# Performance work log

Measured on AMD Instinct MI355X. Metric: run time of the kernel, lower is better.

Reference implementation:

```python
import jax, jax.numpy as jnp
import numpy as np

BIG = 1.0e6  # cost for empty groups
EPS = 1e-6

COST_ACTIVITY = 1.0
COST_GROUP = 1.0
COST_SIZE = 1.0


def setup_inputs() -> dict:
    key = jax.random.key(0)
    k1, k2, k3, k4 = jax.random.split(key, 4)
    bs, Q, C = 256, 512, 128   # batch, num_queries, num_activity_classes
    P, G = 256, 128            # num_persons, num_target_groups
    return {
        "pred_activity_logits": jax.random.normal(k1, (bs, Q, C), dtype=jnp.float32),
        "attention_logits": jax.random.normal(k2, (bs, P, Q), dtype=jnp.float32),
        "tgt_activity_ids": jax.random.randint(k3, (bs, G), 0, C),
        "tgt_group_ids": jax.random.randint(k4, (bs, P), 0, G),
    }


def reference(pred_activity_logits, attention_logits, tgt_activity_ids, tgt_group_ids):
    bs, Q, C = pred_activity_logits.shape
    P = attention_logits.shape[1]
    G = tgt_activity_ids.shape[1]

    # out_attw_b.T -> [Q, P]; log_softmax over dim 0 (queries)
    attw = jnp.transpose(attention_logits, (0, 2, 1))          # [bs, Q, P]
    logP = jax.nn.log_softmax(attw, axis=1)                    # softmax over queries
    P_qn = jnp.exp(logP)
    P_clamped = jnp.clip(P_qn, EPS, 1.0 - EPS)
    lognegP = jnp.log1p(-P_clamped)                            # [bs, Q, P]

    # one-hot grouping target: M[b, p, g] = 1 iff person p in group g
    M = jax.nn.one_hot(tgt_group_ids, G, dtype=logP.dtype)     # [bs, P, G]
    m = M.sum(axis=1)                                          # [bs, G] members per group
    nm = P - m                                                 # nonmembers per group

    # grouping cost: -mean member logP - mean nonmember log(1-P)
    mem_sum = jnp.einsum('bqp,bpg->bqg', logP, M)
    non_sum = jnp.einsum('bqp,bpg->bqg', lognegP, 1.0 - M)
    safe_m = jnp.maximum(m, 1.0)[:, None, :]
    safe_nm = jnp.maximum(nm, 1.0)[:, None, :]
    grouping_cost = -mem_sum / safe_m - non_sum / safe_nm      # [bs, Q, G]

    # size cost: |sum_p P_qn - m| / n_person
    pred_size = P_qn.sum(axis=2)                               # [bs, Q]
    size_cost = jnp.abs(pred_size[:, :, None] - m[:, None, :]) / max(float(P), 1.0)

    empty = (m == 0)[:, None, :]                               # [bs, 1, G]
    grouping_cost = jnp.where(empty, BIG, grouping_cost)
    size_cost = jnp.where(empty, BIG, size_cost)

    # activity cost: cross-entropy of query logits vs each group's activity class
    logq = jax.nn.log_softmax(pred_activity_logits, axis=-1)   # [bs, Q, C]
    idx = jnp.broadcast_to(tgt_activity_ids[:, None, :], (bs, Q, G))
    activity_cost = -jnp.take_along_axis(logq, idx, axis=2)    # [bs, Q, G]

    cost = (COST_GROUP * grouping_cost
            + COST_ACTIVITY * activity_cost
            + COST_SIZE * size_cost)
    return cost
```

## Files before the change

kernel.cpp:

```cpp
#include <hip/hip_runtime.h>

#define BS 256
#define NQ 512
#define NC 128
#define NP 256
#define NG 128
#define TQ 32
#define PTS (NC + 1)
#define BIGC 1.0e6f
#define EPSC 1e-6f


__global__ __launch_bounds__(512) void pre_kernel(const float* __restrict__ att,
                                                  float* __restrict__ lse,
                                                  float* __restrict__ part) {
    __shared__ float attS[32 * NQ];
    __shared__ float invS[32];
    const int t   = threadIdx.x;
    const int blk = blockIdx.x;
    const int b   = blk >> 3;
    const int r   = t >> 4;
    const int p   = (blk & 7) * 32 + r;
    const int sub = t & 15;

    const float4* a4 = (const float4*)(att + ((size_t)(b * NP + p)) * NQ);
    float4 v[8];
#pragma unroll
    for (int i = 0; i < 8; ++i) v[i] = a4[sub + 16 * i];

    float mx = -1e30f;
#pragma unroll
    for (int i = 0; i < 8; ++i)
        mx = fmaxf(mx, fmaxf(fmaxf(v[i].x, v[i].y), fmaxf(v[i].z, v[i].w)));
#pragma unroll
    for (int off = 1; off < 16; off <<= 1) mx = fmaxf(mx, __shfl_xor(mx, off, 64));

    float s = 0.f;
#pragma unroll
    for (int i = 0; i < 8; ++i) {
        v[i].x = __expf(v[i].x - mx); v[i].y = __expf(v[i].y - mx);
        v[i].z = __expf(v[i].z - mx); v[i].w = __expf(v[i].w - mx);
        s += v[i].x + v[i].y + v[i].z + v[i].w;
        *(float4*)(attS + r * NQ + 4 * sub + 64 * i) = v[i];
    }
#pragma unroll
    for (int off = 1; off < 16; off <<= 1) s += __shfl_xor(s, off, 64);
    if (sub == 0) {
        invS[r] = 1.f / s;
        lse[b * NP + p] = mx + __logf(s);
    }
    __syncthreads();

    float sz = 0.f, sl = 0.f;
#pragma unroll 8
    for (int pp = 0; pp < 32; ++pp) {
        const float P = attS[pp * NQ + t] * invS[pp];
        sz += P;
        const float c = fminf(fmaxf(P, EPSC), 1.f - EPSC);
        sl += __logf(1.f - c);
    }
    float* basep = part + (size_t)blk * 2 * NQ;
    basep[t]      = sz;
    basep[NQ + t] = sl;
}

__global__ __launch_bounds__(512, 6) void cost_kernel(
    const float* __restrict__ predAct,
    const float* __restrict__ att,
    const int*   __restrict__ actIds,
    const int*   __restrict__ grpIds,
    const float* __restrict__ lseAtt,
    const float* __restrict__ part,
    float*       __restrict__ out)
{
    __shared__ float wS[NP * TQ];
    __shared__ float pTile[TQ * PTS];
    __shared__ float lseS[NP];
    __shared__ float lseAct[TQ];
    __shared__ float szG[TQ], slG[TQ];
    __shared__ int   gidS[NP];
    __shared__ int   rankS[NP];
    __shared__ int   aidS[NG];
    __shared__ int   cntS[NG];
    __shared__ int   startS[NG];

    const int b  = blockIdx.x >> 4;
    const int q0 = (blockIdx.x & 15) * TQ;
    const int t  = threadIdx.x;

    const int pr  = t >> 3;
    const int qo4 = (t & 7) * 4;
    float4 v[4];
#pragma unroll
    for (int it = 0; it < 4; ++it)
        v[it] = *(const float4*)(att + ((size_t)(b * NP + it * 64 + pr)) * NQ + q0 + qo4);

    const int wv = t >> 6, ln = t & 63;
    float pa0[4], pa1[4];
#pragma unroll
    for (int k = 0; k < 4; ++k) {
        const float* rowp = predAct + ((size_t)(b * NQ + q0 + wv + 8 * k)) * NC;
        pa0[k] = rowp[ln]; pa1[k] = rowp[ln + 64];
    }

    if (t < NP) { lseS[t] = lseAtt[b * NP + t]; gidS[t] = grpIds[b * NP + t]; }
    if (t < NG) { aidS[t] = actIds[b * NG + t]; cntS[t] = 0; }
    if (t < 2 * TQ) {
        const int qo = t & 31, which = t >> 5;
        const float* pb = part + ((size_t)(b * 8)) * 2 * NQ + (size_t)which * NQ + q0 + qo;
        float s = 0.f;
#pragma unroll
        for (int k = 0; k < 8; ++k) s += pb[(size_t)k * 2 * NQ];
        if (which == 0) szG[qo] = s; else slG[qo] = s;
    }
    __syncthreads();

    int myPos = 0;
    if (t < NP) myPos = atomicAdd(&cntS[gidS[t]], 1);
    __syncthreads();

    if (t < 64) {
        const int c0 = cntS[2 * t], c1 = cntS[2 * t + 1];
        const int ps = c0 + c1;
        int s = ps;
#pragma unroll
        for (int off = 1; off < 64; off <<= 1) {
            const int w = __shfl_up(s, off, 64);
            if (t >= off) s += w;
        }
        startS[2 * t]     = s - ps;
        startS[2 * t + 1] = s - ps + c0;
    }
    __syncthreads();
    if (t < NP) rankS[t] = startS[gidS[t]] + myPos;
    __syncthreads();

    #pragma unroll
    for (int it = 0; it < 4; ++it) {
        const int p  = it * 64 + pr;
        const float l = lseS[p];
        const int rr = rankS[p];
        const int m  = cntS[gidS[p]];
        const float im  = 1.f / (float)m;
        const float inm = 1.f / fmaxf((float)(NP - m), 1.f);
        float w[4];
        const float vv[4] = {v[it].x, v[it].y, v[it].z, v[it].w};
#pragma unroll
        for (int j = 0; j < 4; ++j) {
            const float x = vv[j] - l;
            const float e = __expf(x);
            const float c = fminf(fmaxf(e, EPSC), 1.f - EPSC);
            const float ll = __logf(1.f - c);
            w[j] = ll * inm - x * im;
        }
        *(float4*)(wS + rr * TQ + qo4) = *(float4*)w;
    }

#pragma unroll
    for (int k = 0; k < 4; ++k) {
        const int r = wv + 8 * k;
        float mx = fmaxf(pa0[k], pa1[k]);
#pragma unroll
        for (int off = 1; off < 64; off <<= 1) mx = fmaxf(mx, __shfl_xor(mx, off, 64));
        float s = __expf(pa0[k] - mx) + __expf(pa1[k] - mx);
#pragma unroll
        for (int off = 1; off < 64; off <<= 1) s += __shfl_xor(s, off, 64);
        if (ln == 0) lseAct[r] = mx + __logf(s);
        pTile[r * PTS + ln]      = pa0[k];
        pTile[r * PTS + 64 + ln] = pa1[k];
    }
    __syncthreads();

#pragma unroll
    for (int rep = 0; rep < 2; ++rep) {
        const int idx = rep * 512 + t;
        const int qo  = idx & 31;
        const int g4  = (idx >> 5) * 4;
        const float sl = slG[qo], pz = szG[qo], la = lseAct[qo];
        float res[4];
#pragma unroll
        for (int j = 0; j < 4; ++j) {
            const int g  = g4 + j;
            const int m  = cntS[g];
            const int st = startS[g];
            float s = 0.f;
            for (int i = 0; i < m; ++i) s += wS[(st + i) * TQ + qo];
            const float mf  = (float)m;
            const float nmf = fmaxf((float)(NP - m), 1.f);
            float grp = s - sl / nmf;
            float szc = fabsf(pz - mf) * (1.f / (float)NP);
            if (m == 0) { grp = BIGC; szc = BIGC; }
            const float av = pTile[qo * PTS + aidS[g]];
            res[j] = grp + (la - av) + szc;
        }
        *(float4*)(out + ((size_t)(b * NQ + q0 + qo)) * NG + g4) = *(float4*)res;
    }
}

extern "C" void kernel_launch(void* const* d_in, const int* in_sizes, int n_in,
                              void* d_out, int out_size, void* d_ws, size_t ws_size,
                              hipStream_t stream) {
    const float* predAct = (const float*)d_in[0];
    const float* att     = (const float*)d_in[1];
    const int*   actIds  = (const int*)d_in[2];
    const int*   grpIds  = (const int*)d_in[3];
    float*       out     = (float*)d_out;
    float*       lse     = (float*)d_ws;
    float*       part    = lse + (size_t)BS * NP;

    pre_kernel<<<BS * 8, 512, 0, stream>>>(att, lse, part);
    cost_kernel<<<BS * (NQ / TQ), 512, 0, stream>>>(predAct, att, actIds, grpIds, lse, part, out);
}
```

Baseline: 313.7 us.

## Replace per-group member loops with prefix-sum differences and halve pre_kernel LDS

The cost kernel now computes an exclusive prefix sum over the group-sorted weight rows in shared memory, so each group's member sum is a difference of two entries rather than a variable-length loop. Group start and count are packed into one int, and several shared arrays are merged into a scratch buffer to cut LDS use. The pre kernel stages probabilities in two halves through a 16-row buffer, normalising in registers, which halves its LDS and allows more resident blocks. Prefix-sum differences can add float cancellation error, and the pre kernel gains extra barriers.

```diff
diff --git a/kernel.cpp b/kernel.cpp
--- a/kernel.cpp
+++ b/kernel.cpp
@@ -11,11 +11,10 @@
 #define EPSC 1e-6f
 
 
-__global__ __launch_bounds__(512) void pre_kernel(const float* __restrict__ att,
-                                                  float* __restrict__ lse,
-                                                  float* __restrict__ part) {
-    __shared__ float attS[32 * NQ];
-    __shared__ float invS[32];
+__global__ __launch_bounds__(512, 8) void pre_kernel(const float* __restrict__ att,
+                                                     float* __restrict__ lse,
+                                                     float* __restrict__ part) {
+    __shared__ float attS[16 * NQ];
     const int t   = threadIdx.x;
     const int blk = blockIdx.x;
     const int b   = blk >> 3;
@@ -41,24 +40,45 @@
         v[i].x = __expf(v[i].x - mx); v[i].y = __expf(v[i].y - mx);
         v[i].z = __expf(v[i].z - mx); v[i].w = __expf(v[i].w - mx);
         s += v[i].x + v[i].y + v[i].z + v[i].w;
-        *(float4*)(attS + r * NQ + 4 * sub + 64 * i) = v[i];
     }
 #pragma unroll
     for (int off = 1; off < 16; off <<= 1) s += __shfl_xor(s, off, 64);
-    if (sub == 0) {
-        invS[r] = 1.f / s;
-        lse[b * NP + p] = mx + __logf(s);
-    }
-    __syncthreads();
+    const float inv = 1.f / s;
+    if (sub == 0) lse[b * NP + p] = mx + __logf(s);
+#pragma unroll
+    for (int i = 0; i < 8; ++i) {
+        v[i].x *= inv; v[i].y *= inv; v[i].z *= inv; v[i].w *= inv;
+    }
 
     float sz = 0.f, sl = 0.f;
-#pragma unroll 8
-    for (int pp = 0; pp < 32; ++pp) {
-        const float P = attS[pp * NQ + t] * invS[pp];
+    if (r < 16) {
+#pragma unroll
+        for (int i = 0; i < 8; ++i)
+            *(float4*)(attS + r * NQ + 4 * sub + 64 * i) = v[i];
+    }
+    __syncthreads();
+#pragma unroll
+    for (int pp = 0; pp < 16; ++pp) {
+        const float P = attS[pp * NQ + t];
         sz += P;
         const float c = fminf(fmaxf(P, EPSC), 1.f - EPSC);
         sl += __logf(1.f - c);
     }
+    __syncthreads();
+    if (r >= 16) {
+#pragma unroll
+        for (int i = 0; i < 8; ++i)
+            *(float4*)(attS + (r - 16) * NQ + 4 * sub + 64 * i) = v[i];
+    }
+    __syncthreads();
+#pragma unroll
+    for (int pp = 0; pp < 16; ++pp) {
+        const float P = attS[pp * NQ + t];
+        sz += P;
+        const float c = fminf(fmaxf(P, EPSC), 1.f - EPSC);
+        sl += __logf(1.f - c);
+    }
+
     float* basep = part + (size_t)blk * 2 * NQ;
     basep[t]      = sz;
     basep[NQ + t] = sl;
@@ -73,16 +93,17 @@
     const float* __restrict__ part,
     float*       __restrict__ out)
 {
-    __shared__ float wS[NP * TQ];
+    __shared__ float wS[(NP + 1) * TQ];
     __shared__ float pTile[TQ * PTS];
-    __shared__ float lseS[NP];
+    __shared__ float scratch[512];
     __shared__ float lseAct[TQ];
     __shared__ float szG[TQ], slG[TQ];
-    __shared__ int   gidS[NP];
-    __shared__ int   rankS[NP];
     __shared__ int   aidS[NG];
     __shared__ int   cntS[NG];
-    __shared__ int   startS[NG];
+
+    float* lseS  = scratch;
+    int*   prS   = (int*)(scratch + 256);
+    float* scanP = scratch;
 
     const int b  = blockIdx.x >> 4;
     const int q0 = (blockIdx.x & 15) * TQ;
@@ -103,7 +124,7 @@
         pa0[k] = rowp[ln]; pa1[k] = rowp[ln + 64];
     }
 
-    if (t < NP) { lseS[t] = lseAtt[b * NP + t]; gidS[t] = grpIds[b * NP + t]; }
+    if (t < NP) { lseS[t] = lseAtt[b * NP + t]; prS[t] = grpIds[b * NP + t]; }
     if (t < NG) { aidS[t] = actIds[b * NG + t]; cntS[t] = 0; }
     if (t < 2 * TQ) {
         const int qo = t & 31, which = t >> 5;
@@ -116,7 +137,7 @@
     __syncthreads();
 
     int myPos = 0;
-    if (t < NP) myPos = atomicAdd(&cntS[gidS[t]], 1);
+    if (t < NP) myPos = atomicAdd(&cntS[prS[t]], 1);
     __syncthreads();
 
     if (t < 64) {
@@ -128,19 +149,25 @@
             const int w = __shfl_up(s, off, 64);
             if (t >= off) s += w;
         }
-        startS[2 * t]     = s - ps;
-        startS[2 * t + 1] = s - ps + c0;
-    }
-    __syncthreads();
-    if (t < NP) rankS[t] = startS[gidS[t]] + myPos;
-    __syncthreads();
-
-    #pragma unroll
+        const int e = s - ps;
+        cntS[2 * t]     = e | (c0 << 16);
+        cntS[2 * t + 1] = (e + c0) | (c1 << 16);
+    }
+    __syncthreads();
+    if (t < NP) {
+        const int g  = prS[t];
+        const int cs = cntS[g];
+        prS[t] = ((cs & 0xffff) + myPos) | (cs & 0xffff0000);
+    }
+    __syncthreads();
+
+#pragma unroll
     for (int it = 0; it < 4; ++it) {
         const int p  = it * 64 + pr;
         const float l = lseS[p];
-        const int rr = rankS[p];
-        const int m  = cntS[gidS[p]];
+        const int pk = prS[p];
+        const int rr = pk & 0xffff;
+        const int m  = pk >> 16;
         const float im  = 1.f / (float)m;
         const float inm = 1.f / fmaxf((float)(NP - m), 1.f);
         float w[4];
@@ -171,6 +198,29 @@
     }
     __syncthreads();
 
+    {
+        const int cq = t & 31;
+        const int ck = t >> 5;
+        float pv[16];
+        float run = 0.f;
+#pragma unroll
+        for (int i = 0; i < 16; ++i) {
+            pv[i] = run;
+            run += wS[(16 * ck + i) * TQ + cq];
+        }
+        scanP[ck * 32 + cq] = run;
+        __syncthreads();
+        float offs = 0.f;
+#pragma unroll
+        for (int j = 0; j < 15; ++j)
+            if (j < ck) offs += scanP[j * 32 + cq];
+#pragma unroll
+        for (int i = 0; i < 16; ++i)
+            wS[(16 * ck + i) * TQ + cq] = offs + pv[i];
+        if (ck == 15) wS[NP * TQ + cq] = offs + run;
+    }
+    __syncthreads();
+
 #pragma unroll
     for (int rep = 0; rep < 2; ++rep) {
         const int idx = rep * 512 + t;
@@ -181,13 +231,13 @@
 #pragma unroll
         for (int j = 0; j < 4; ++j) {
             const int g  = g4 + j;
-            const int m  = cntS[g];
-            const int st = startS[g];
-            float s = 0.f;
-            for (int i = 0; i < m; ++i) s += wS[(st + i) * TQ + qo];
+            const int cs = cntS[g];
+            const int m  = cs >> 16;
+            const int st = cs & 0xffff;
+            const float ms = wS[(st + m) * TQ + qo] - wS[st * TQ + qo];
             const float mf  = (float)m;
             const float nmf = fmaxf((float)(NP - m), 1.f);
-            float grp = s - sl / nmf;
+            float grp = ms - sl / nmf;
             float szc = fabsf(pz - mf) * (1.f / (float)NP);
             if (m == 0) { grp = BIGC; szc = BIGC; }
             const float av = pTile[qo * PTS + aidS[g]];
```

Result: faster. 299.3 us (-4.6%).
